# Kernel tuning notes

Measured on AMD Instinct MI355X. Metric: run time of the kernel, lower is better.

Reference implementation:

```python
import jax, jax.numpy as jnp
import numpy as np

EMBED_DIM = 1024
NUM_HEAD = 16
HEAD_DIM = EMBED_DIM // NUM_HEAD


def setup_inputs() -> dict:
    key = jax.random.key(0)
    ks = jax.random.split(key, 9)
    B, S, D = 2, 2048, EMBED_DIM
    scale = 1.0 / np.sqrt(D)
    x = jax.random.normal(ks[0], (B, S, D), dtype=jnp.float32)
    Wq = jax.random.normal(ks[1], (D, D), dtype=jnp.float32) * scale
    bq = jnp.zeros((D,), jnp.float32)
    Wk = jax.random.normal(ks[2], (D, D), dtype=jnp.float32) * scale
    bk = jnp.zeros((D,), jnp.float32)
    Wv = jax.random.normal(ks[3], (D, D), dtype=jnp.float32) * scale
    bv = jnp.zeros((D,), jnp.float32)
    Wfc = jax.random.normal(ks[4], (D, D), dtype=jnp.float32) * scale
    bfc = jnp.zeros((D,), jnp.float32)
    return {"x": x, "Wq": Wq, "bq": bq, "Wk": Wk, "bk": bk,
            "Wv": Wv, "bv": bv, "Wfc": Wfc, "bfc": bfc}


def _split_heads(t):
    B, S, D = t.shape
    return t.reshape(B, S, NUM_HEAD, HEAD_DIM).transpose(0, 2, 1, 3)  # b nh s hd


def reference(x, Wq, bq, Wk, bk, Wv, bv, Wfc, bfc):
    # torch nn.Linear: y = x @ W.T + b
    q = _split_heads(x @ Wq.T + bq)   # [b, nh, s, hd]
    k = _split_heads(x @ Wk.T + bk)   # [b, nh, s, hd]
    v = _split_heads(x @ Wv.T + bv)   # [b, nh, s, hd]
    # Gram matrix K^T K per (batch, head): [b, nh, hd, hd]
    gram = jnp.einsum('bnsh,bnsk->bnhk', k, k)
    gram_inv = jnp.linalg.inv(gram)
    # score = Q (K^T K)^{-1} K^T : [b, nh, s, s]
    q_proj = jnp.einsum('bnsh,bnhk->bnsk', q, gram_inv)
    score = jnp.einsum('bnsk,bntk->bnst', q_proj, k)
    attn = jax.nn.softmax(score / jnp.sqrt(jnp.float32(EMBED_DIM)), axis=-1)
    out = jnp.einsum('bnst,bnth->bnsh', attn, v)  # [b, nh, s, hd]
    B, _, S, _ = out.shape
    out = out.transpose(0, 2, 1, 3).reshape(B, S, EMBED_DIM)
    return out @ Wfc.T + bfc
```

## Files before the change

### kernel.cpp

```cpp
#include <hip/hip_runtime.h>
#include <cstddef>
#include <cstdint>

#define S_LEN 2048
#define NHEAD 16
#define HDIM  64
#define EMB   1024
#define MROWS 4096

typedef short bf16x8 __attribute__((ext_vector_type(8)));
typedef float f32x4 __attribute__((ext_vector_type(4)));

__device__ __forceinline__ unsigned short f2bf(float f) {
  union { float f; unsigned u; } v; v.f = f;
  return (unsigned short)((v.u + 0x8000u) >> 16);
}
__device__ __forceinline__ unsigned pack2bf(float a, float b) {
  union { float f; unsigned u; } x, y; x.f = a; y.f = b;
  return ((x.u + 0x8000u) >> 16) | ((y.u + 0x8000u) & 0xFFFF0000u);
}

__device__ __forceinline__ f32x4 fzero() {
  f32x4 z = {0.0f, 0.0f, 0.0f, 0.0f};
  return z;
}

__global__ __launch_bounds__(256) void cast_kernel(
    const float* __restrict__ x, const float* __restrict__ Wq,
    const float* __restrict__ Wk, const float* __restrict__ Wv,
    const float* __restrict__ Wfc, unsigned short* __restrict__ dst)
{
  size_t idx8 = (size_t)(blockIdx.x * 256 + threadIdx.x) * 8;
  unsigned seg = (unsigned)(idx8 >> 20);
  const float* src;
  size_t off;
  if (seg < 4) { src = x; off = idx8; }
  else {
    const float* w4[4] = {Wq, Wk, Wv, Wfc};
    src = w4[seg - 4];
    off = idx8 & 0xFFFFFu;
  }
  float4 a = *(const float4*)&src[off];
  float4 b = *(const float4*)&src[off + 4];
  uint4 p;
  p.x = pack2bf(a.x, a.y);
  p.y = pack2bf(a.z, a.w);
  p.z = pack2bf(b.x, b.y);
  p.w = pack2bf(b.z, b.w);
  *(uint4*)&dst[idx8] = p;
}

__global__ __launch_bounds__(256) void gemm_qkv(
    const unsigned short* __restrict__ A, const unsigned short* __restrict__ Wall,
    const float* __restrict__ bq, const float* __restrict__ bk,
    const float* __restrict__ bv, unsigned short* __restrict__ Qhd,
    unsigned short* __restrict__ Khd, unsigned short* __restrict__ KTd,
    unsigned short* __restrict__ VTd)
{
  __shared__ short As[128][40];
  __shared__ short Bs[128][40];
  const int z = blockIdx.z;
  const unsigned short* B = Wall + (size_t)z * 1048576;
  const float* bias = (z == 0) ? bq : (z == 1) ? bk : bv;
  unsigned short* Yh = (z == 0) ? Qhd : (z == 1) ? Khd : nullptr;
  unsigned short* Yt = (z == 1) ? KTd : (z == 2) ? VTd : nullptr;
  const int K = EMB;
  const int t = threadIdx.x;
  const int lane = t & 63, w = t >> 6;
  const int quad = lane >> 4, l16 = lane & 15;
  const int wr = w >> 1, wc = w & 1;
  const int m0 = blockIdx.y * 128, n0 = blockIdx.x * 128;
  const int sr = t >> 2, sk = (t & 3) * 8;

  f32x4 acc[4][4];
#pragma unroll
  for (int i = 0; i < 4; ++i)
#pragma unroll
    for (int j = 0; j < 4; ++j) acc[i][j] = fzero();

  float4 pa0 = *(const float4*)&A[(size_t)(m0 + sr) * K + sk];
  float4 pa1 = *(const float4*)&A[(size_t)(m0 + 64 + sr) * K + sk];
  float4 pb0 = *(const float4*)&B[(size_t)(n0 + sr) * K + sk];
  float4 pb1 = *(const float4*)&B[(size_t)(n0 + 64 + sr) * K + sk];

  for (int k0 = 0; k0 < K; k0 += 32) {
    __syncthreads();
    *(float4*)&As[sr][sk] = pa0;
    *(float4*)&As[64 + sr][sk] = pa1;
    *(float4*)&Bs[sr][sk] = pb0;
    *(float4*)&Bs[64 + sr][sk] = pb1;
    __syncthreads();
    if (k0 + 32 < K) {
      pa0 = *(const float4*)&A[(size_t)(m0 + sr) * K + k0 + 32 + sk];
      pa1 = *(const float4*)&A[(size_t)(m0 + 64 + sr) * K + k0 + 32 + sk];
      pb0 = *(const float4*)&B[(size_t)(n0 + sr) * K + k0 + 32 + sk];
      pb1 = *(const float4*)&B[(size_t)(n0 + 64 + sr) * K + k0 + 32 + sk];
    }
    bf16x8 af[4], bfr[4];
#pragma unroll
    for (int i = 0; i < 4; ++i)
      af[i] = *(const bf16x8*)&As[64 * wr + 16 * i + l16][quad * 8];
#pragma unroll
    for (int j = 0; j < 4; ++j)
      bfr[j] = *(const bf16x8*)&Bs[64 * wc + 16 * j + l16][quad * 8];
#pragma unroll
    for (int i = 0; i < 4; ++i)
#pragma unroll
      for (int j = 0; j < 4; ++j)
        acc[i][j] = __builtin_amdgcn_mfma_f32_16x16x32_bf16(af[i], bfr[j], acc[i][j], 0, 0, 0);
  }

#pragma unroll
  for (int i = 0; i < 4; ++i) {
    int mb = m0 + 64 * wr + 16 * i + quad * 4;
#pragma unroll
    for (int j = 0; j < 4; ++j) {
      int n = n0 + 64 * wc + 16 * j + l16;
      float bvv = bias[n];
      int h = n >> 6, d = n & 63;
      if (Yh) {
#pragma unroll
        for (int r = 0; r < 4; ++r) {
          int m = mb + r;
          int b = m >> 11, s = m & 2047;
          Yh[((size_t)(b * NHEAD + h)) * 131072 + (size_t)s * 64 + d] =
              f2bf(acc[i][j][r] + bvv);
        }
      }
      if (Yt) {
        int b = mb >> 11, s = mb & 2047;
        uint2 pk;
        pk.x = pack2bf(acc[i][j][0] + bvv, acc[i][j][1] + bvv);
        pk.y = pack2bf(acc[i][j][2] + bvv, acc[i][j][3] + bvv);
        *(uint2*)&Yt[((size_t)(b * NHEAD + h)) * 131072 + (size_t)d * S_LEN + s] = pk;
      }
    }
  }
}

__global__ __launch_bounds__(256) void gemm_fc(
    const unsigned short* __restrict__ A, const unsigned short* __restrict__ B,
    const float* __restrict__ bias, float* __restrict__ Yf)
{
  __shared__ short As[128][40];
  __shared__ short Bs[128][40];
  const int K = EMB, N = EMB;
  const int t = threadIdx.x;
  const int lane = t & 63, w = t >> 6;
  const int quad = lane >> 4, l16 = lane & 15;
  const int wr = w >> 1, wc = w & 1;
  const int m0 = blockIdx.y * 128, n0 = blockIdx.x * 128;
  const int sr = t >> 2, sk = (t & 3) * 8;

  f32x4 acc[4][4];
#pragma unroll
  for (int i = 0; i < 4; ++i)
#pragma unroll
    for (int j = 0; j < 4; ++j) acc[i][j] = fzero();

  float4 pa0 = *(const float4*)&A[(size_t)(m0 + sr) * K + sk];
  float4 pa1 = *(const float4*)&A[(size_t)(m0 + 64 + sr) * K + sk];
  float4 pb0 = *(const float4*)&B[(size_t)(n0 + sr) * K + sk];
  float4 pb1 = *(const float4*)&B[(size_t)(n0 + 64 + sr) * K + sk];

  for (int k0 = 0; k0 < K; k0 += 32) {
    __syncthreads();
    *(float4*)&As[sr][sk] = pa0;
    *(float4*)&As[64 + sr][sk] = pa1;
    *(float4*)&Bs[sr][sk] = pb0;
    *(float4*)&Bs[64 + sr][sk] = pb1;
    __syncthreads();
    if (k0 + 32 < K) {
      pa0 = *(const float4*)&A[(size_t)(m0 + sr) * K + k0 + 32 + sk];
      pa1 = *(const float4*)&A[(size_t)(m0 + 64 + sr) * K + k0 + 32 + sk];
      pb0 = *(const float4*)&B[(size_t)(n0 + sr) * K + k0 + 32 + sk];
      pb1 = *(const float4*)&B[(size_t)(n0 + 64 + sr) * K + k0 + 32 + sk];
    }
    bf16x8 af[4], bfr[4];
#pragma unroll
    for (int i = 0; i < 4; ++i)
      af[i] = *(const bf16x8*)&As[64 * wr + 16 * i + l16][quad * 8];
#pragma unroll
    for (int j = 0; j < 4; ++j)
      bfr[j] = *(const bf16x8*)&Bs[64 * wc + 16 * j + l16][quad * 8];
#pragma unroll
    for (int i = 0; i < 4; ++i)
#pragma unroll
      for (int j = 0; j < 4; ++j)
        acc[i][j] = __builtin_amdgcn_mfma_f32_16x16x32_bf16(af[i], bfr[j], acc[i][j], 0, 0, 0);
  }

#pragma unroll
  for (int i = 0; i < 4; ++i) {
    int mb = m0 + 64 * wr + 16 * i + quad * 4;
#pragma unroll
    for (int j = 0; j < 4; ++j) {
      int n = n0 + 64 * wc + 16 * j + l16;
      float bvv = bias[n];
#pragma unroll
      for (int r = 0; r < 4; ++r)
        Yf[(size_t)(mb + r) * N + n] = acc[i][j][r] + bvv;
    }
  }
}

__global__ __launch_bounds__(256) void gram_mfma(
    const unsigned short* __restrict__ KTh, float* __restrict__ gram_p)
{
  __shared__ short KTs[64][136];
  const int t = threadIdx.x;
  const int lane = t & 63, w = t >> 6;
  const int quad = lane >> 4, l16 = lane & 15;
  const int bh = blockIdx.x >> 2, part = blockIdx.x & 3;
  const unsigned short* Kb = KTh + (size_t)bh * 131072 + part * 512;

  f32x4 gacc[4];
#pragma unroll
  for (int j = 0; j < 4; ++j) gacc[j] = fzero();

  const int rv = t >> 4, cv = (t & 15) * 8;
  for (int st = 0; st < 4; ++st) {
    float4 vv[4];
#pragma unroll
    for (int r = 0; r < 4; ++r)
      vv[r] = *(const float4*)&Kb[(size_t)(rv + 16 * r) * S_LEN + st * 128 + cv];
    __syncthreads();
#pragma unroll
    for (int r = 0; r < 4; ++r)
      *(float4*)&KTs[rv + 16 * r][cv] = vv[r];
    __syncthreads();
#pragma unroll
    for (int c = 0; c < 4; ++c) {
      bf16x8 ai = *(const bf16x8*)&KTs[16 * w + l16][32 * c + quad * 8];
#pragma unroll
      for (int jb = 0; jb < 4; ++jb) {
        bf16x8 bj = *(const bf16x8*)&KTs[16 * jb + l16][32 * c + quad * 8];
        gacc[jb] = __builtin_amdgcn_mfma_f32_16x16x32_bf16(ai, bj, gacc[jb], 0, 0, 0);
      }
    }
  }
#pragma unroll
  for (int jb = 0; jb < 4; ++jb)
#pragma unroll
    for (int r = 0; r < 4; ++r)
      gram_p[(size_t)blockIdx.x * 4096 +
             (size_t)(16 * w + quad * 4 + r) * 64 + 16 * jb + l16] = gacc[jb][r];
}

__global__ __launch_bounds__(256) void inv_kernel(
    const float* __restrict__ gram_p, unsigned short* __restrict__ ginv)
{
  __shared__ float As[64][68];
  __shared__ float prow[2][64];
  __shared__ float fcol[2][64];
  const int bh = blockIdx.x;
  const int t = threadIdx.x;
  const int r = t >> 2;
  const int c0 = (t & 3) * 16;
  const float* G = gram_p + (size_t)bh * 4 * 4096;

  float4 g[4];
#pragma unroll
  for (int jj = 0; jj < 4; ++jj) {
    int off = r * 64 + c0 + 4 * jj;
    float4 s0 = *(const float4*)&G[off];
    float4 s1 = *(const float4*)&G[4096 + off];
    float4 s2 = *(const float4*)&G[8192 + off];
    float4 s3 = *(const float4*)&G[12288 + off];
    g[jj].x = (s0.x + s1.x) + (s2.x + s3.x);
    g[jj].y = (s0.y + s1.y) + (s2.y + s3.y);
    g[jj].z = (s0.z + s1.z) + (s2.z + s3.z);
    g[jj].w = (s0.w + s1.w) + (s2.w + s3.w);
    *(float4*)&As[r][c0 + 4 * jj] = g[jj];
  }
  if (c0 == 0) fcol[0][r] = g[0].x;
  if (r == 0) {
#pragma unroll
    for (int jj = 0; jj < 4; ++jj) *(float4*)&prow[0][c0 + 4 * jj] = g[jj];
  }
  __syncthreads();

  for (int k = 0; k < 64; ++k) {
    const int kb = k & 1;
    const float f = fcol[kb][r];
    const float ip = 1.0f / fcol[kb][k];
    const float fi = f * ip;
    const bool pr = (r == k);
    float4 nv[4];
#pragma unroll
    for (int jj = 0; jj < 4; ++jj) {
      float4 a = *(const float4*)&As[r][c0 + 4 * jj];
      float4 p = *(const float4*)&prow[kb][c0 + 4 * jj];
      float4 o;
      if (pr) {
        o.x = p.x * ip; o.y = p.y * ip; o.z = p.z * ip; o.w = p.w * ip;
      } else {
        o.x = fmaf(-fi, p.x, a.x); o.y = fmaf(-fi, p.y, a.y);
        o.z = fmaf(-fi, p.z, a.z); o.w = fmaf(-fi, p.w, a.w);
      }
      const int cb = c0 + 4 * jj;
      const float kv = pr ? ip : -fi;
      if (cb == k) o.x = kv;
      if (cb + 1 == k) o.y = kv;
      if (cb + 2 == k) o.z = kv;
      if (cb + 3 == k) o.w = kv;
      *(float4*)&As[r][c0 + 4 * jj] = o;
      nv[jj] = o;
    }
    if (k < 63) {
      const int nk = k + 1, nb = nk & 1;
      if (nk >= c0 && nk < c0 + 16) fcol[nb][r] = As[r][nk];
      if (r == nk) {
#pragma unroll
        for (int jj = 0; jj < 4; ++jj) *(float4*)&prow[nb][c0 + 4 * jj] = nv[jj];
      }
    }
    __syncthreads();
  }

  unsigned short* O = ginv + (size_t)bh * 4096;
#pragma unroll
  for (int jj = 0; jj < 4; ++jj) {
    float4 v = *(const float4*)&As[r][c0 + 4 * jj];
    uint2 pk;
    pk.x = pack2bf(v.x, v.y);
    pk.y = pack2bf(v.z, v.w);
    *(uint2*)&O[r * 64 + c0 + 4 * jj] = pk;
  }
}

__global__ __launch_bounds__(256) void flash_mfma(
    const unsigned short* __restrict__ Qh, const unsigned short* __restrict__ Kh,
    const unsigned short* __restrict__ VTh, const unsigned short* __restrict__ Ginv,
    unsigned short* __restrict__ AO)
{
  __shared__ short Qps[64 * 72];
  __shared__ short Ps[2][64 * 72];
  __shared__ float Lred[4][64];
  const int t = threadIdx.x;
  const int lane = t & 63, w = t >> 6;
  const int quad = lane >> 4, l16 = lane & 15;
  const int qt = blockIdx.x, bh = blockIdx.y;
  const unsigned short* Qb = Qh + (size_t)bh * 131072;
  const unsigned short* Kb = Kh + (size_t)bh * 131072;
  const unsigned short* Vb = VTh + (size_t)bh * 131072;
  const unsigned short* Gb = Ginv + (size_t)bh * 4096;

  {
    bf16x8 aq[2];
#pragma unroll
    for (int c = 0; c < 2; ++c)
      aq[c] = *(const bf16x8*)&Qb[(size_t)(qt * 64 + 16 * w + l16) * 64 + 32 * c + 8 * quad];
    f32x4 qacc[4];
#pragma unroll
    for (int nb = 0; nb < 4; ++nb) qacc[nb] = fzero();
#pragma unroll
    for (int c = 0; c < 2; ++c) {
#pragma unroll
      for (int nb = 0; nb < 4; ++nb) {
        bf16x8 bg = *(const bf16x8*)&Gb[(size_t)(16 * nb + l16) * 64 + 32 * c + 8 * quad];
        qacc[nb] = __builtin_amdgcn_mfma_f32_16x16x32_bf16(aq[c], bg, qacc[nb], 0, 0, 0);
      }
    }
#pragma unroll
    for (int nb = 0; nb < 4; ++nb)
#pragma unroll
      for (int r = 0; r < 4; ++r)
        Qps[(16 * w + 4 * quad + r) * 72 + 16 * nb + l16] =
            (short)f2bf(qacc[nb][r] * 0.03125f);
  }
  __syncthreads();

  f32x4 oacc[4];
#pragma unroll
  for (int qb = 0; qb < 4; ++qb) oacc[qb] = fzero();
  float lsum[4] = {0.0f, 0.0f, 0.0f, 0.0f};

  for (int kt = 0; kt < 32; ++kt) {
    bf16x8 ak[2];
#pragma unroll
    for (int c = 0; c < 2; ++c)
      ak[c] = *(const bf16x8*)&Kb[(size_t)(kt * 64 + 16 * w + l16) * 64 + 32 * c + 8 * quad];
    f32x4 sacc[4];
#pragma unroll
    for (int qb = 0; qb < 4; ++qb) sacc[qb] = fzero();
#pragma unroll
    for (int c = 0; c < 2; ++c) {
#pragma unroll
      for (int qb = 0; qb < 4; ++qb) {
        bf16x8 bq = *(const bf16x8*)&Qps[(16 * qb + l16) * 72 + 32 * c + 8 * quad];
        sacc[qb] = __builtin_amdgcn_mfma_f32_16x16x32_bf16(ak[c], bq, sacc[qb], 0, 0, 0);
      }
    }
    short* Pbuf = &Ps[kt & 1][0];
#pragma unroll
    for (int qb = 0; qb < 4; ++qb) {
      float e0 = __expf(sacc[qb][0]);
      float e1 = __expf(sacc[qb][1]);
      float e2 = __expf(sacc[qb][2]);
      float e3 = __expf(sacc[qb][3]);
      lsum[qb] += (e0 + e1) + (e2 + e3);
      uint2 pk;
      pk.x = pack2bf(e0, e1);
      pk.y = pack2bf(e2, e3);
      *(uint2*)&Pbuf[(16 * qb + l16) * 72 + 16 * w + 4 * quad] = pk;
    }
    __syncthreads();

    bf16x8 av[2];
#pragma unroll
    for (int c = 0; c < 2; ++c)
      av[c] = *(const bf16x8*)&Vb[(size_t)(16 * w + l16) * S_LEN + kt * 64 + 32 * c + 8 * quad];
#pragma unroll
    for (int c = 0; c < 2; ++c) {
#pragma unroll
      for (int qb = 0; qb < 4; ++qb) {
        bf16x8 bp = *(const bf16x8*)&Pbuf[(16 * qb + l16) * 72 + 32 * c + 8 * quad];
        oacc[qb] = __builtin_amdgcn_mfma_f32_16x16x32_bf16(av[c], bp, oacc[qb], 0, 0, 0);
      }
    }
  }

#pragma unroll
  for (int qb = 0; qb < 4; ++qb) {
    lsum[qb] += __shfl_xor(lsum[qb], 16, 64);
    lsum[qb] += __shfl_xor(lsum[qb], 32, 64);
  }
  if (lane < 16)
#pragma unroll
    for (int qb = 0; qb < 4; ++qb) Lred[w][qb * 16 + l16] = lsum[qb];
  __syncthreads();
  if (t < 64)
    Lred[0][t] = 1.0f / (Lred[0][t] + Lred[1][t] + Lred[2][t] + Lred[3][t]);
  __syncthreads();

  const int b = bh >> 4, h = bh & 15;
#pragma unroll
  for (int qb = 0; qb < 4; ++qb) {
    float li = Lred[0][16 * qb + l16];
    int s = qt * 64 + 16 * qb + l16;
    size_t base = (size_t)b * S_LEN * EMB + (size_t)s * EMB + h * 64 + 16 * w + 4 * quad;
#pragma unroll
    for (int r = 0; r < 4; ++r)
      AO[base + r] = f2bf(oacc[qb][r] * li);
  }
}

extern "C" void kernel_launch(void* const* d_in, const int* in_sizes, int n_in,
                              void* d_out, int out_size, void* d_ws, size_t ws_size,
                              hipStream_t stream) {
  (void)in_sizes; (void)n_in; (void)out_size; (void)ws_size;
  const float* x   = (const float*)d_in[0];
  const float* Wq  = (const float*)d_in[1];
  const float* bq  = (const float*)d_in[2];
  const float* Wk  = (const float*)d_in[3];
  const float* bk  = (const float*)d_in[4];
  const float* Wv  = (const float*)d_in[5];
  const float* bv  = (const float*)d_in[6];
  const float* Wfc = (const float*)d_in[7];
  const float* bfc = (const float*)d_in[8];
  float* out = (float*)d_out;

  unsigned short* xb   = (unsigned short*)d_ws;
  unsigned short* Wqb  = xb + (size_t)4194304;
  unsigned short* Wfcb = Wqb + 3 * 1048576;
  unsigned short* Qhd  = Wfcb + 1048576;
  unsigned short* Khd  = Qhd + 4194304;
  unsigned short* KTd  = Khd + 4194304;
  unsigned short* VTd  = KTd + 4194304;
  unsigned short* AOd  = VTd + 4194304;
  float* gram_p        = (float*)(AOd + 4194304);
  unsigned short* ginv = (unsigned short*)(gram_p + 524288);

  cast_kernel<<<4096, 256, 0, stream>>>(x, Wq, Wk, Wv, Wfc, xb);
  gemm_qkv<<<dim3(8, 32, 3), 256, 0, stream>>>(xb, Wqb, bq, bk, bv,
                                               Qhd, Khd, KTd, VTd);
  gram_mfma<<<128, 256, 0, stream>>>(KTd, gram_p);
  inv_kernel<<<32, 256, 0, stream>>>(gram_p, ginv);
  flash_mfma<<<dim3(S_LEN / 64, 32), 256, 0, stream>>>(Qhd, Khd, VTd, ginv, AOd);
  gemm_fc<<<dim3(8, 32), 256, 0, stream>>>(AOd, Wfcb, bfc, out);
}
```

Before: 285.9 us.

## Use direct global-to-LDS loads in GEMMs and pipeline flash attention loads

Both projection GEMMs now stage A and B tiles through global_load_lds straight into unpadded shared memory, replacing the register-prefetch path. This removes the register round trip and VGPR pressure, but drops the padding and the prefetch overlap, so LDS bank conflicts may appear. The flash kernel now prefetches the next K tile and the V tile earlier, keeps Q fragments in registers, and folds log2(e) into the Q scale so it can use exp2f. It also packs the output stores, adds an occupancy hint, and remaps the grid so blocks sharing a head run together.

```diff
diff --git a/kernel.cpp b/kernel.cpp
--- a/kernel.cpp
+++ b/kernel.cpp
@@ -23,6 +23,12 @@
 __device__ __forceinline__ f32x4 fzero() {
   f32x4 z = {0.0f, 0.0f, 0.0f, 0.0f};
   return z;
+}
+
+__device__ __forceinline__ void gl_lds16(const void* g, void* l) {
+  __builtin_amdgcn_global_load_lds(
+      (const __attribute__((address_space(1))) void*)g,
+      (__attribute__((address_space(3))) void*)l, 16, 0, 0);
 }
 
 __global__ __launch_bounds__(256) void cast_kernel(
@@ -57,8 +63,8 @@
     unsigned short* __restrict__ Khd, unsigned short* __restrict__ KTd,
     unsigned short* __restrict__ VTd)
 {
-  __shared__ short As[128][40];
-  __shared__ short Bs[128][40];
+  __shared__ short As[128][32];
+  __shared__ short Bs[128][32];
   const int z = blockIdx.z;
   const unsigned short* B = Wall + (size_t)z * 1048576;
   const float* bias = (z == 0) ? bq : (z == 1) ? bk : bv;
@@ -70,7 +76,10 @@
   const int quad = lane >> 4, l16 = lane & 15;
   const int wr = w >> 1, wc = w & 1;
   const int m0 = blockIdx.y * 128, n0 = blockIdx.x * 128;
-  const int sr = t >> 2, sk = (t & 3) * 8;
+  const int srow = 32 * w + (lane >> 2);
+  const int scol = (lane & 3) * 8;
+  short* ldsA = &As[0][0] + 1024 * w;
+  short* ldsB = &Bs[0][0] + 1024 * w;
 
   f32x4 acc[4][4];
 #pragma unroll
@@ -78,24 +87,13 @@
 #pragma unroll
     for (int j = 0; j < 4; ++j) acc[i][j] = fzero();
 
-  float4 pa0 = *(const float4*)&A[(size_t)(m0 + sr) * K + sk];
-  float4 pa1 = *(const float4*)&A[(size_t)(m0 + 64 + sr) * K + sk];
-  float4 pb0 = *(const float4*)&B[(size_t)(n0 + sr) * K + sk];
-  float4 pb1 = *(const float4*)&B[(size_t)(n0 + 64 + sr) * K + sk];
-
   for (int k0 = 0; k0 < K; k0 += 32) {
     __syncthreads();
-    *(float4*)&As[sr][sk] = pa0;
-    *(float4*)&As[64 + sr][sk] = pa1;
-    *(float4*)&Bs[sr][sk] = pb0;
-    *(float4*)&Bs[64 + sr][sk] = pb1;
-    __syncthreads();
-    if (k0 + 32 < K) {
-      pa0 = *(const float4*)&A[(size_t)(m0 + sr) * K + k0 + 32 + sk];
-      pa1 = *(const float4*)&A[(size_t)(m0 + 64 + sr) * K + k0 + 32 + sk];
-      pb0 = *(const float4*)&B[(size_t)(n0 + sr) * K + k0 + 32 + sk];
-      pb1 = *(const float4*)&B[(size_t)(n0 + 64 + sr) * K + k0 + 32 + sk];
-    }
+    gl_lds16(&A[(size_t)(m0 + srow) * K + k0 + scol], ldsA);
+    gl_lds16(&A[(size_t)(m0 + srow + 16) * K + k0 + scol], ldsA + 512);
+    gl_lds16(&B[(size_t)(n0 + srow) * K + k0 + scol], ldsB);
+    gl_lds16(&B[(size_t)(n0 + srow + 16) * K + k0 + scol], ldsB + 512);
+    __syncthreads();
     bf16x8 af[4], bfr[4];
 #pragma unroll
     for (int i = 0; i < 4; ++i)
@@ -142,15 +140,18 @@
     const unsigned short* __restrict__ A, const unsigned short* __restrict__ B,
     const float* __restrict__ bias, float* __restrict__ Yf)
 {
-  __shared__ short As[128][40];
-  __shared__ short Bs[128][40];
+  __shared__ short As[128][32];
+  __shared__ short Bs[128][32];
   const int K = EMB, N = EMB;
   const int t = threadIdx.x;
   const int lane = t & 63, w = t >> 6;
   const int quad = lane >> 4, l16 = lane & 15;
   const int wr = w >> 1, wc = w & 1;
   const int m0 = blockIdx.y * 128, n0 = blockIdx.x * 128;
-  const int sr = t >> 2, sk = (t & 3) * 8;
+  const int srow = 32 * w + (lane >> 2);
+  const int scol = (lane & 3) * 8;
+  short* ldsA = &As[0][0] + 1024 * w;
+  short* ldsB = &Bs[0][0] + 1024 * w;
 
   f32x4 acc[4][4];
 #pragma unroll
@@ -158,24 +159,13 @@
 #pragma unroll
     for (int j = 0; j < 4; ++j) acc[i][j] = fzero();
 
-  float4 pa0 = *(const float4*)&A[(size_t)(m0 + sr) * K + sk];
-  float4 pa1 = *(const float4*)&A[(size_t)(m0 + 64 + sr) * K + sk];
-  float4 pb0 = *(const float4*)&B[(size_t)(n0 + sr) * K + sk];
-  float4 pb1 = *(const float4*)&B[(size_t)(n0 + 64 + sr) * K + sk];
-
   for (int k0 = 0; k0 < K; k0 += 32) {
     __syncthreads();
-    *(float4*)&As[sr][sk] = pa0;
-    *(float4*)&As[64 + sr][sk] = pa1;
-    *(float4*)&Bs[sr][sk] = pb0;
-    *(float4*)&Bs[64 + sr][sk] = pb1;
-    __syncthreads();
-    if (k0 + 32 < K) {
-      pa0 = *(const float4*)&A[(size_t)(m0 + sr) * K + k0 + 32 + sk];
-      pa1 = *(const float4*)&A[(size_t)(m0 + 64 + sr) * K + k0 + 32 + sk];
-      pb0 = *(const float4*)&B[(size_t)(n0 + sr) * K + k0 + 32 + sk];
-      pb1 = *(const float4*)&B[(size_t)(n0 + 64 + sr) * K + k0 + 32 + sk];
-    }
+    gl_lds16(&A[(size_t)(m0 + srow) * K + k0 + scol], ldsA);
+    gl_lds16(&A[(size_t)(m0 + srow + 16) * K + k0 + scol], ldsA + 512);
+    gl_lds16(&B[(size_t)(n0 + srow) * K + k0 + scol], ldsB);
+    gl_lds16(&B[(size_t)(n0 + srow + 16) * K + k0 + scol], ldsB + 512);
+    __syncthreads();
     bf16x8 af[4], bfr[4];
 #pragma unroll
     for (int i = 0; i < 4; ++i)
@@ -329,7 +319,7 @@
   }
 }
 
-__global__ __launch_bounds__(256) void flash_mfma(
+__global__ __launch_bounds__(256, 4) void flash_mfma(
     const unsigned short* __restrict__ Qh, const unsigned short* __restrict__ Kh,
     const unsigned short* __restrict__ VTh, const unsigned short* __restrict__ Ginv,
     unsigned short* __restrict__ AO)
@@ -340,12 +330,18 @@
   const int t = threadIdx.x;
   const int lane = t & 63, w = t >> 6;
   const int quad = lane >> 4, l16 = lane & 15;
-  const int qt = blockIdx.x, bh = blockIdx.y;
+  const int id = blockIdx.x;
+  const int qt = (id >> 3) & 31;
+  const int bh = ((id >> 8) << 3) | (id & 7);
   const unsigned short* Qb = Qh + (size_t)bh * 131072;
   const unsigned short* Kb = Kh + (size_t)bh * 131072;
   const unsigned short* Vb = VTh + (size_t)bh * 131072;
   const unsigned short* Gb = Ginv + (size_t)bh * 4096;
 
+  bf16x8 ak[2];
+#pragma unroll
+  for (int c = 0; c < 2; ++c)
+    ak[c] = *(const bf16x8*)&Kb[(size_t)(16 * w + l16) * 64 + 32 * c + 8 * quad];
   {
     bf16x8 aq[2];
 #pragma unroll
@@ -362,14 +358,22 @@
         qacc[nb] = __builtin_amdgcn_mfma_f32_16x16x32_bf16(aq[c], bg, qacc[nb], 0, 0, 0);
       }
     }
+    const float cs = 0.04508422e0f;
 #pragma unroll
     for (int nb = 0; nb < 4; ++nb)
 #pragma unroll
       for (int r = 0; r < 4; ++r)
         Qps[(16 * w + 4 * quad + r) * 72 + 16 * nb + l16] =
-            (short)f2bf(qacc[nb][r] * 0.03125f);
+            (short)f2bf(qacc[nb][r] * cs);
   }
   __syncthreads();
+
+  bf16x8 bqf[2][4];
+#pragma unroll
+  for (int c = 0; c < 2; ++c)
+#pragma unroll
+    for (int qb = 0; qb < 4; ++qb)
+      bqf[c][qb] = *(const bf16x8*)&Qps[(16 * qb + l16) * 72 + 32 * c + 8 * quad];
 
   f32x4 oacc[4];
 #pragma unroll
@@ -377,28 +381,32 @@
   float lsum[4] = {0.0f, 0.0f, 0.0f, 0.0f};
 
   for (int kt = 0; kt < 32; ++kt) {
-    bf16x8 ak[2];
+    bf16x8 av[2];
 #pragma unroll
     for (int c = 0; c < 2; ++c)
-      ak[c] = *(const bf16x8*)&Kb[(size_t)(kt * 64 + 16 * w + l16) * 64 + 32 * c + 8 * quad];
+      av[c] = *(const bf16x8*)&Vb[(size_t)(16 * w + l16) * S_LEN + kt * 64 + 32 * c + 8 * quad];
+
     f32x4 sacc[4];
 #pragma unroll
     for (int qb = 0; qb < 4; ++qb) sacc[qb] = fzero();
 #pragma unroll
-    for (int c = 0; c < 2; ++c) {
-#pragma unroll
-      for (int qb = 0; qb < 4; ++qb) {
-        bf16x8 bq = *(const bf16x8*)&Qps[(16 * qb + l16) * 72 + 32 * c + 8 * quad];
-        sacc[qb] = __builtin_amdgcn_mfma_f32_16x16x32_bf16(ak[c], bq, sacc[qb], 0, 0, 0);
-      }
-    }
+    for (int c = 0; c < 2; ++c)
+#pragma unroll
+      for (int qb = 0; qb < 4; ++qb)
+        sacc[qb] = __builtin_amdgcn_mfma_f32_16x16x32_bf16(ak[c], bqf[c][qb], sacc[qb], 0, 0, 0);
+
+    const int nk = (kt + 1) & 31;
+#pragma unroll
+    for (int c = 0; c < 2; ++c)
+      ak[c] = *(const bf16x8*)&Kb[(size_t)(nk * 64 + 16 * w + l16) * 64 + 32 * c + 8 * quad];
+
     short* Pbuf = &Ps[kt & 1][0];
 #pragma unroll
     for (int qb = 0; qb < 4; ++qb) {
-      float e0 = __expf(sacc[qb][0]);
-      float e1 = __expf(sacc[qb][1]);
-      float e2 = __expf(sacc[qb][2]);
-      float e3 = __expf(sacc[qb][3]);
+      float e0 = exp2f(sacc[qb][0]);
+      float e1 = exp2f(sacc[qb][1]);
+      float e2 = exp2f(sacc[qb][2]);
+      float e3 = exp2f(sacc[qb][3]);
       lsum[qb] += (e0 + e1) + (e2 + e3);
       uint2 pk;
       pk.x = pack2bf(e0, e1);
@@ -407,18 +415,13 @@
     }
     __syncthreads();
 
-    bf16x8 av[2];
 #pragma unroll
     for (int c = 0; c < 2; ++c)
-      av[c] = *(const bf16x8*)&Vb[(size_t)(16 * w + l16) * S_LEN + kt * 64 + 32 * c + 8 * quad];
-#pragma unroll
-    for (int c = 0; c < 2; ++c) {
 #pragma unroll
       for (int qb = 0; qb < 4; ++qb) {
         bf16x8 bp = *(const bf16x8*)&Pbuf[(16 * qb + l16) * 72 + 32 * c + 8 * quad];
         oacc[qb] = __builtin_amdgcn_mfma_f32_16x16x32_bf16(av[c], bp, oacc[qb], 0, 0, 0);
       }
-    }
   }
 
 #pragma unroll
@@ -440,9 +443,10 @@
     float li = Lred[0][16 * qb + l16];
     int s = qt * 64 + 16 * qb + l16;
     size_t base = (size_t)b * S_LEN * EMB + (size_t)s * EMB + h * 64 + 16 * w + 4 * quad;
-#pragma unroll
-    for (int r = 0; r < 4; ++r)
-      AO[base + r] = f2bf(oacc[qb][r] * li);
+    uint2 pk;
+    pk.x = pack2bf(oacc[qb][0] * li, oacc[qb][1] * li);
+    pk.y = pack2bf(oacc[qb][2] * li, oacc[qb][3] * li);
+    *(uint2*)&AO[base] = pk;
   }
 }
 
@@ -477,6 +481,6 @@
                                                Qhd, Khd, KTd, VTd);
   gram_mfma<<<128, 256, 0, stream>>>(KTd, gram_p);
   inv_kernel<<<32, 256, 0, stream>>>(gram_p, ginv);
-  flash_mfma<<<dim3(S_LEN / 64, 32), 256, 0, stream>>>(Qhd, Khd, VTd, ginv, AOd);
+  flash_mfma<<<1024, 256, 0, stream>>>(Qhd, Khd, VTd, ginv, AOd);
   gemm_fc<<<dim3(8, 32), 256, 0, stream>>>(AOd, Wfcb, bfc, out);
 }
```

After: 292.5 us. 1.02x slower.

## Fuse gram and inverse kernels, widen flash tiles, shrink fc tiles

Applied to the files above, without the earlier changes.

Merges the gram-matrix and inverse kernels into one launch, dropping the partial-gram workspace round trip at the cost of only 32 blocks computing the full gram each. The flash kernel now processes 128 keys per iteration, uses exp2 with a log2e-folded scale, remaps blocks so heads group together, sets an occupancy hint, and packs output stores. The fc GEMM uses 128x64 tiles to launch twice as many blocks. The gram stage loses its 4-way split parallelism, which may lengthen that stage.

```diff
diff --git a/kernel.cpp b/kernel.cpp
--- a/kernel.cpp
+++ b/kernel.cpp
@@ -143,50 +143,47 @@
     const float* __restrict__ bias, float* __restrict__ Yf)
 {
   __shared__ short As[128][40];
-  __shared__ short Bs[128][40];
+  __shared__ short Bs[64][40];
   const int K = EMB, N = EMB;
   const int t = threadIdx.x;
   const int lane = t & 63, w = t >> 6;
   const int quad = lane >> 4, l16 = lane & 15;
   const int wr = w >> 1, wc = w & 1;
-  const int m0 = blockIdx.y * 128, n0 = blockIdx.x * 128;
+  const int m0 = blockIdx.y * 128, n0 = blockIdx.x * 64;
   const int sr = t >> 2, sk = (t & 3) * 8;
 
-  f32x4 acc[4][4];
+  f32x4 acc[4][2];
 #pragma unroll
   for (int i = 0; i < 4; ++i)
 #pragma unroll
-    for (int j = 0; j < 4; ++j) acc[i][j] = fzero();
+    for (int j = 0; j < 2; ++j) acc[i][j] = fzero();
 
   float4 pa0 = *(const float4*)&A[(size_t)(m0 + sr) * K + sk];
   float4 pa1 = *(const float4*)&A[(size_t)(m0 + 64 + sr) * K + sk];
   float4 pb0 = *(const float4*)&B[(size_t)(n0 + sr) * K + sk];
-  float4 pb1 = *(const float4*)&B[(size_t)(n0 + 64 + sr) * K + sk];
 
   for (int k0 = 0; k0 < K; k0 += 32) {
     __syncthreads();
     *(float4*)&As[sr][sk] = pa0;
     *(float4*)&As[64 + sr][sk] = pa1;
-    *(float4*)&Bs[sr][sk] = pb0;
-    *(float4*)&Bs[64 + sr][sk] = pb1;
+    if (sr < 64) *(float4*)&Bs[sr][sk] = pb0;
     __syncthreads();
     if (k0 + 32 < K) {
       pa0 = *(const float4*)&A[(size_t)(m0 + sr) * K + k0 + 32 + sk];
       pa1 = *(const float4*)&A[(size_t)(m0 + 64 + sr) * K + k0 + 32 + sk];
       pb0 = *(const float4*)&B[(size_t)(n0 + sr) * K + k0 + 32 + sk];
-      pb1 = *(const float4*)&B[(size_t)(n0 + 64 + sr) * K + k0 + 32 + sk];
-    }
-    bf16x8 af[4], bfr[4];
+    }
+    bf16x8 af[4], bfr[2];
 #pragma unroll
     for (int i = 0; i < 4; ++i)
       af[i] = *(const bf16x8*)&As[64 * wr + 16 * i + l16][quad * 8];
 #pragma unroll
-    for (int j = 0; j < 4; ++j)
-      bfr[j] = *(const bf16x8*)&Bs[64 * wc + 16 * j + l16][quad * 8];
+    for (int j = 0; j < 2; ++j)
+      bfr[j] = *(const bf16x8*)&Bs[32 * wc + 16 * j + l16][quad * 8];
 #pragma unroll
     for (int i = 0; i < 4; ++i)
 #pragma unroll
-      for (int j = 0; j < 4; ++j)
+      for (int j = 0; j < 2; ++j)
         acc[i][j] = __builtin_amdgcn_mfma_f32_16x16x32_bf16(af[i], bfr[j], acc[i][j], 0, 0, 0);
   }
 
@@ -194,8 +191,8 @@
   for (int i = 0; i < 4; ++i) {
     int mb = m0 + 64 * wr + 16 * i + quad * 4;
 #pragma unroll
-    for (int j = 0; j < 4; ++j) {
-      int n = n0 + 64 * wc + 16 * j + l16;
+    for (int j = 0; j < 2; ++j) {
+      int n = n0 + 32 * wc + 16 * j + l16;
       float bvv = bias[n];
 #pragma unroll
       for (int r = 0; r < 4; ++r)
@@ -204,22 +201,24 @@
   }
 }
 
-__global__ __launch_bounds__(256) void gram_mfma(
-    const unsigned short* __restrict__ KTh, float* __restrict__ gram_p)
+__global__ __launch_bounds__(256) void graminv_kernel(
+    const unsigned short* __restrict__ KTh, unsigned short* __restrict__ ginv)
 {
   __shared__ short KTs[64][136];
+  __shared__ float As[64][68];
+  __shared__ float prow[2][64];
+  __shared__ float fcol[2][64];
   const int t = threadIdx.x;
   const int lane = t & 63, w = t >> 6;
   const int quad = lane >> 4, l16 = lane & 15;
-  const int bh = blockIdx.x >> 2, part = blockIdx.x & 3;
-  const unsigned short* Kb = KTh + (size_t)bh * 131072 + part * 512;
+  const int bh = blockIdx.x;
+  const unsigned short* Kb = KTh + (size_t)bh * 131072;
 
   f32x4 gacc[4];
 #pragma unroll
   for (int j = 0; j < 4; ++j) gacc[j] = fzero();
-
   const int rv = t >> 4, cv = (t & 15) * 8;
-  for (int st = 0; st < 4; ++st) {
+  for (int st = 0; st < 16; ++st) {
     float4 vv[4];
 #pragma unroll
     for (int r = 0; r < 4; ++r)
@@ -243,40 +242,16 @@
   for (int jb = 0; jb < 4; ++jb)
 #pragma unroll
     for (int r = 0; r < 4; ++r)
-      gram_p[(size_t)blockIdx.x * 4096 +
-             (size_t)(16 * w + quad * 4 + r) * 64 + 16 * jb + l16] = gacc[jb][r];
-}
-
-__global__ __launch_bounds__(256) void inv_kernel(
-    const float* __restrict__ gram_p, unsigned short* __restrict__ ginv)
-{
-  __shared__ float As[64][68];
-  __shared__ float prow[2][64];
-  __shared__ float fcol[2][64];
-  const int bh = blockIdx.x;
-  const int t = threadIdx.x;
+      As[16 * w + 4 * quad + r][16 * jb + l16] = gacc[jb][r];
+  __syncthreads();
+
   const int r = t >> 2;
   const int c0 = (t & 3) * 16;
-  const float* G = gram_p + (size_t)bh * 4 * 4096;
-
-  float4 g[4];
-#pragma unroll
-  for (int jj = 0; jj < 4; ++jj) {
-    int off = r * 64 + c0 + 4 * jj;
-    float4 s0 = *(const float4*)&G[off];
-    float4 s1 = *(const float4*)&G[4096 + off];
-    float4 s2 = *(const float4*)&G[8192 + off];
-    float4 s3 = *(const float4*)&G[12288 + off];
-    g[jj].x = (s0.x + s1.x) + (s2.x + s3.x);
-    g[jj].y = (s0.y + s1.y) + (s2.y + s3.y);
-    g[jj].z = (s0.z + s1.z) + (s2.z + s3.z);
-    g[jj].w = (s0.w + s1.w) + (s2.w + s3.w);
-    *(float4*)&As[r][c0 + 4 * jj] = g[jj];
-  }
-  if (c0 == 0) fcol[0][r] = g[0].x;
+  if (c0 == 0) fcol[0][r] = As[r][0];
   if (r == 0) {
 #pragma unroll
-    for (int jj = 0; jj < 4; ++jj) *(float4*)&prow[0][c0 + 4 * jj] = g[jj];
+    for (int jj = 0; jj < 4; ++jj)
+      *(float4*)&prow[0][c0 + 4 * jj] = *(const float4*)&As[0][c0 + 4 * jj];
   }
   __syncthreads();
 
@@ -329,18 +304,20 @@
   }
 }
 
-__global__ __launch_bounds__(256) void flash_mfma(
+__global__ __launch_bounds__(256, 4) void flash_mfma(
     const unsigned short* __restrict__ Qh, const unsigned short* __restrict__ Kh,
     const unsigned short* __restrict__ VTh, const unsigned short* __restrict__ Ginv,
     unsigned short* __restrict__ AO)
 {
   __shared__ short Qps[64 * 72];
-  __shared__ short Ps[2][64 * 72];
+  __shared__ short Ps[64 * 136];
   __shared__ float Lred[4][64];
   const int t = threadIdx.x;
   const int lane = t & 63, w = t >> 6;
   const int quad = lane >> 4, l16 = lane & 15;
-  const int qt = blockIdx.x, bh = blockIdx.y;
+  const int id = blockIdx.x;
+  const int qt = (id >> 3) & 31;
+  const int bh = ((id >> 8) << 3) | (id & 7);
   const unsigned short* Qb = Qh + (size_t)bh * 131072;
   const unsigned short* Kb = Kh + (size_t)bh * 131072;
   const unsigned short* Vb = VTh + (size_t)bh * 131072;
@@ -362,12 +339,13 @@
         qacc[nb] = __builtin_amdgcn_mfma_f32_16x16x32_bf16(aq[c], bg, qacc[nb], 0, 0, 0);
       }
     }
+    const float cs = 0.04508422e0f;
 #pragma unroll
     for (int nb = 0; nb < 4; ++nb)
 #pragma unroll
       for (int r = 0; r < 4; ++r)
         Qps[(16 * w + 4 * quad + r) * 72 + 16 * nb + l16] =
-            (short)f2bf(qacc[nb][r] * 0.03125f);
+            (short)f2bf(qacc[nb][r] * cs);
   }
   __syncthreads();
 
@@ -376,49 +354,73 @@
   for (int qb = 0; qb < 4; ++qb) oacc[qb] = fzero();
   float lsum[4] = {0.0f, 0.0f, 0.0f, 0.0f};
 
-  for (int kt = 0; kt < 32; ++kt) {
-    bf16x8 ak[2];
-#pragma unroll
-    for (int c = 0; c < 2; ++c)
-      ak[c] = *(const bf16x8*)&Kb[(size_t)(kt * 64 + 16 * w + l16) * 64 + 32 * c + 8 * quad];
-    f32x4 sacc[4];
-#pragma unroll
-    for (int qb = 0; qb < 4; ++qb) sacc[qb] = fzero();
-#pragma unroll
-    for (int c = 0; c < 2; ++c) {
-#pragma unroll
-      for (int qb = 0; qb < 4; ++qb) {
-        bf16x8 bq = *(const bf16x8*)&Qps[(16 * qb + l16) * 72 + 32 * c + 8 * quad];
-        sacc[qb] = __builtin_amdgcn_mfma_f32_16x16x32_bf16(ak[c], bq, sacc[qb], 0, 0, 0);
-      }
-    }
-    short* Pbuf = &Ps[kt & 1][0];
+  for (int kt = 0; kt < 16; ++kt) {
+    bf16x8 ak0[2], ak1[2], av[4];
+#pragma unroll
+    for (int c = 0; c < 2; ++c)
+      ak0[c] = *(const bf16x8*)&Kb[(size_t)(kt * 128 + 16 * w + l16) * 64 + 32 * c + 8 * quad];
+#pragma unroll
+    for (int c = 0; c < 2; ++c)
+      ak1[c] = *(const bf16x8*)&Kb[(size_t)(kt * 128 + 64 + 16 * w + l16) * 64 + 32 * c + 8 * quad];
+#pragma unroll
+    for (int c = 0; c < 4; ++c)
+      av[c] = *(const bf16x8*)&Vb[(size_t)(16 * w + l16) * S_LEN + kt * 128 + 32 * c + 8 * quad];
+
+    bf16x8 bqf[2][4];
+#pragma unroll
+    for (int c = 0; c < 2; ++c)
+#pragma unroll
+      for (int qb = 0; qb < 4; ++qb)
+        bqf[c][qb] = *(const bf16x8*)&Qps[(16 * qb + l16) * 72 + 32 * c + 8 * quad];
+
+    f32x4 sa[4], sb[4];
+#pragma unroll
+    for (int qb = 0; qb < 4; ++qb) { sa[qb] = fzero(); sb[qb] = fzero(); }
+#pragma unroll
+    for (int c = 0; c < 2; ++c)
+#pragma unroll
+      for (int qb = 0; qb < 4; ++qb)
+        sa[qb] = __builtin_amdgcn_mfma_f32_16x16x32_bf16(ak0[c], bqf[c][qb], sa[qb], 0, 0, 0);
+#pragma unroll
+    for (int c = 0; c < 2; ++c)
+#pragma unroll
+      for (int qb = 0; qb < 4; ++qb)
+        sb[qb] = __builtin_amdgcn_mfma_f32_16x16x32_bf16(ak1[c], bqf[c][qb], sb[qb], 0, 0, 0);
+
 #pragma unroll
     for (int qb = 0; qb < 4; ++qb) {
-      float e0 = __expf(sacc[qb][0]);
-      float e1 = __expf(sacc[qb][1]);
-      float e2 = __expf(sacc[qb][2]);
-      float e3 = __expf(sacc[qb][3]);
+      float e0 = exp2f(sa[qb][0]);
+      float e1 = exp2f(sa[qb][1]);
+      float e2 = exp2f(sa[qb][2]);
+      float e3 = exp2f(sa[qb][3]);
       lsum[qb] += (e0 + e1) + (e2 + e3);
       uint2 pk;
       pk.x = pack2bf(e0, e1);
       pk.y = pack2bf(e2, e3);
-      *(uint2*)&Pbuf[(16 * qb + l16) * 72 + 16 * w + 4 * quad] = pk;
-    }
-    __syncthreads();
-
-    bf16x8 av[2];
-#pragma unroll
-    for (int c = 0; c < 2; ++c)
-      av[c] = *(const bf16x8*)&Vb[(size_t)(16 * w + l16) * S_LEN + kt * 64 + 32 * c + 8 * quad];
-#pragma unroll
-    for (int c = 0; c < 2; ++c) {
+      *(uint2*)&Ps[(16 * qb + l16) * 136 + 16 * w + 4 * quad] = pk;
+    }
+#pragma unroll
+    for (int qb = 0; qb < 4; ++qb) {
+      float e0 = exp2f(sb[qb][0]);
+      float e1 = exp2f(sb[qb][1]);
+      float e2 = exp2f(sb[qb][2]);
+      float e3 = exp2f(sb[qb][3]);
+      lsum[qb] += (e0 + e1) + (e2 + e3);
+      uint2 pk;
+      pk.x = pack2bf(e0, e1);
+      pk.y = pack2bf(e2, e3);
+      *(uint2*)&Ps[(16 * qb + l16) * 136 + 64 + 16 * w + 4 * quad] = pk;
+    }
+    __syncthreads();
+
+#pragma unroll
+    for (int c = 0; c < 4; ++c)
 #pragma unroll
       for (int qb = 0; qb < 4; ++qb) {
-        bf16x8 bp = *(const bf16x8*)&Pbuf[(16 * qb + l16) * 72 + 32 * c + 8 * quad];
+        bf16x8 bp = *(const bf16x8*)&Ps[(16 * qb + l16) * 136 + 32 * c + 8 * quad];
         oacc[qb] = __builtin_amdgcn_mfma_f32_16x16x32_bf16(av[c], bp, oacc[qb], 0, 0, 0);
       }
-    }
+    __syncthreads();
   }
 
 #pragma unroll
@@ -440,9 +442,10 @@
     float li = Lred[0][16 * qb + l16];
     int s = qt * 64 + 16 * qb + l16;
     size_t base = (size_t)b * S_LEN * EMB + (size_t)s * EMB + h * 64 + 16 * w + 4 * quad;
-#pragma unroll
-    for (int r = 0; r < 4; ++r)
-      AO[base + r] = f2bf(oacc[qb][r] * li);
+    uint2 pk;
+    pk.x = pack2bf(oacc[qb][0] * li, oacc[qb][1] * li);
+    pk.y = pack2bf(oacc[qb][2] * li, oacc[qb][3] * li);
+    *(uint2*)&AO[base] = pk;
   }
 }
 
@@ -469,14 +472,12 @@
   unsigned short* KTd  = Khd + 4194304;
   unsigned short* VTd  = KTd + 4194304;
   unsigned short* AOd  = VTd + 4194304;
-  float* gram_p        = (float*)(AOd + 4194304);
-  unsigned short* ginv = (unsigned short*)(gram_p + 524288);
+  unsigned short* ginv = AOd + 4194304;
 
   cast_kernel<<<4096, 256, 0, stream>>>(x, Wq, Wk, Wv, Wfc, xb);
   gemm_qkv<<<dim3(8, 32, 3), 256, 0, stream>>>(xb, Wqb, bq, bk, bv,
                                                Qhd, Khd, KTd, VTd);
-  gram_mfma<<<128, 256, 0, stream>>>(KTd, gram_p);
-  inv_kernel<<<32, 256, 0, stream>>>(gram_p, ginv);
-  flash_mfma<<<dim3(S_LEN / 64, 32), 256, 0, stream>>>(Qhd, Khd, VTd, ginv, AOd);
-  gemm_fc<<<dim3(8, 32), 256, 0, stream>>>(AOd, Wfcb, bfc, out);
-}
+  graminv_kernel<<<32, 256, 0, stream>>>(KTd, ginv);
+  flash_mfma<<<1024, 256, 0, stream>>>(Qhd, Khd, VTd, ginv, AOd);
+  gemm_fc<<<dim3(16, 32), 256, 0, stream>>>(AOd, Wfcb, bfc, out);
+}
```

After: 305.4 us. 6.8% more time.
